# Performance work log

Measured on AMD Instinct MI355X. Metric: run time of the kernel, lower is better.

The kernel has to match this reference:

```python
import jax, jax.numpy as jnp
import numpy as np

N_CH = 62
F_DIM = 16
T_DIM = 32
B_DIM = 256
N_NODES = B_DIM * N_CH  # 15872
E_DIM = 200000
SEQ = T_DIM * F_DIM  # 512


def setup_inputs() -> dict:
    key = jax.random.key(0)
    ks = iter(jax.random.split(key, 40))
    s = 0.05
    inp = {}
    inp['x'] = jax.random.normal(next(ks), (N_NODES, F_DIM, T_DIM), dtype=jnp.float32)
    inp['edge_index'] = jax.random.randint(next(ks), (T_DIM, 2, E_DIM), 0, N_NODES, dtype=jnp.int64)
    inp['edge_weight'] = jax.random.uniform(next(ks), (T_DIM, E_DIM), dtype=jnp.float32)
    inp['batch'] = jax.random.randint(next(ks), (T_DIM, N_NODES), 0, B_DIM, dtype=jnp.int64)
    # ChebConv params (K=2): lins have no bias, single bias added at end
    for p in ['c1', 'c2']:
        inp[p + '_w0'] = jax.random.normal(next(ks), (F_DIM, F_DIM), dtype=jnp.float32) * s
        inp[p + '_w1'] = jax.random.normal(next(ks), (F_DIM, F_DIM), dtype=jnp.float32) * s
        inp[p + '_b'] = jnp.zeros((F_DIM,), jnp.float32)
    # LSTM params (torch gate order i,f,g,o); fold b_ih+b_hh into one bias
    for name, i_dim, h_dim in [('l1', N_CH, 64), ('l2', 64, 128), ('l3', 128, 256)]:
        inp[name + '_wih'] = jax.random.normal(next(ks), (4 * h_dim, i_dim), dtype=jnp.float32) * s
        inp[name + '_whh'] = jax.random.normal(next(ks), (4 * h_dim, h_dim), dtype=jnp.float32) * s
        inp[name + '_b'] = jnp.zeros((4 * h_dim,), jnp.float32)
    # MLP head
    for name, i_dim, o_dim in [('fc1', SEQ * 256, 256), ('fc2', 256, 128), ('fc3', 128, 64), ('fc4', 64, 4)]:
        inp[name + '_w'] = jax.random.normal(next(ks), (i_dim, o_dim), dtype=jnp.float32) * s
        inp[name + '_b'] = jnp.zeros((o_dim,), jnp.float32)
    return inp


def _cheb(x, src, dst, w, w0, w1, b):
    # PyG ChebConv K=2, sym norm, lambda_max=2: Tx1 = -D^{-1/2} A D^{-1/2} x
    n = x.shape[0]
    deg = jax.ops.segment_sum(w, src, num_segments=n)
    dinv = jnp.where(deg > 0, jax.lax.rsqrt(deg), 0.0)
    norm = -dinv[src] * w * dinv[dst]
    tx1 = jax.ops.segment_sum(norm[:, None] * x[src], dst, num_segments=n)
    return x @ w0 + tx1 @ w1 + b


def _lstm(x, wih, whh, b):
    # x: [B, S, I] -> [B, S, H], batch_first, zero init state
    bsz, _, _ = x.shape
    h_dim = whh.shape[1]
    xg = x @ wih.T + b  # precompute input gates [B, S, 4H]
    def step(carry, xt):
        h, c = carry
        g = xt + h @ whh.T
        i, f, gg, o = jnp.split(g, 4, axis=-1)
        c = jax.nn.sigmoid(f) * c + jax.nn.sigmoid(i) * jnp.tanh(gg)
        h = jax.nn.sigmoid(o) * jnp.tanh(c)
        return (h, c), h
    h0 = jnp.zeros((bsz, h_dim), x.dtype)
    _, hs = jax.lax.scan(step, (h0, h0), jnp.swapaxes(xg, 0, 1))
    return jnp.swapaxes(hs, 0, 1)


def reference(x, edge_index, edge_weight, batch,
              c1_w0, c1_w1, c1_b, c2_w0, c2_w1, c2_b,
              l1_wih, l1_whh, l1_b, l2_wih, l2_whh, l2_b, l3_wih, l3_whh, l3_b,
              fc1_w, fc1_b, fc2_w, fc2_b, fc3_w, fc3_b, fc4_w, fc4_b):
    def per_t(xt, ei, w):
        h = _cheb(xt, ei[0], ei[1], w, c1_w0, c1_w1, c1_b)
        h = jax.nn.leaky_relu(h, 0.01)
        return _cheb(h, ei[0], ei[1], w, c2_w0, c2_w1, c2_b)
    xt_first = jnp.moveaxis(x, -1, 0)  # [T, N, F]
    h = jax.vmap(per_t)(xt_first, edge_index, edge_weight)  # [T, N, F]
    xc = jnp.moveaxis(h, 0, -1)  # [N, F, T]
    xc = xc.reshape(B_DIM, N_CH, F_DIM, T_DIM)
    xc = jnp.transpose(xc, (0, 3, 2, 1))  # [B, T, F, 62]
    xc = xc.reshape(B_DIM, T_DIM * F_DIM, N_CH)  # [B, S, 62]
    h = _lstm(xc, l1_wih, l1_whh, l1_b)
    h = _lstm(h, l2_wih, l2_whh, l2_b)
    h = _lstm(h, l3_wih, l3_whh, l3_b)
    z = h.reshape(B_DIM, -1)  # [B, S*256]
    z = jax.nn.relu(z @ fc1_w + fc1_b)
    z = jax.nn.relu(z @ fc2_w + fc2_b)
    z = jax.nn.relu(z @ fc3_w + fc3_b)
    return z @ fc4_w + fc4_b
```

## Files before the change

### kernel.cpp

```cpp
#include <hip/hip_runtime.h>
#include <cstdint>
#include <cstddef>


#define T_DIM 32
#define F_DIMC 16
#define NNODE 15872
#define EDGES 200000
#define BATCH 256
#define SEQL 512
#define TN (T_DIM * NNODE)
#define TE (T_DIM * EDGES)

typedef unsigned short ushortT;
typedef __bf16 bf16_t;
typedef bf16_t bf16x8 __attribute__((ext_vector_type(8)));
typedef float f32x4 __attribute__((ext_vector_type(4)));

__device__ __forceinline__ ushortT f2bf(float f) {
  union { float f; unsigned u; } v; v.f = f;
  unsigned u = v.u;
  u += 0x7fffu + ((u >> 16) & 1u);
  return (ushortT)(u >> 16);
}
__device__ __forceinline__ float fsig(float x) { return 1.0f / (1.0f + __expf(-x)); }
__device__ __forceinline__ float ftanh(float x) {
  float e = __expf(2.0f * x);
  return 1.0f - 2.0f / (e + 1.0f);
}
#define PIN(v) asm volatile("" : "+v"(v))

__device__ __forceinline__ void bar_sync() {
  asm volatile("s_waitcnt lgkmcnt(0)\n\ts_barrier" ::: "memory");
  __builtin_amdgcn_sched_barrier(0);
}

__global__ void k_wprep(const float* __restrict__ w1i, const float* __restrict__ w1h,
                        const float* __restrict__ w2i, const float* __restrict__ w2h,
                        const float* __restrict__ w3i, const float* __restrict__ w3h,
                        ushortT* __restrict__ Wcat) {
  int id = blockIdx.x * 256 + threadIdx.x;
  if (id >= 524288) return;
  float v;
  if (id < 32768) {
    int g = id >> 7, k = id & 127;
    v = (k < 62) ? w1i[g * 62 + k] : ((k >= 64) ? w1h[g * 64 + (k - 64)] : 0.0f);
  } else if (id < 131072) {
    int j = id - 32768; int g = j / 192, k = j % 192;
    v = (k < 64) ? w2i[g * 64 + k] : w2h[g * 128 + (k - 64)];
  } else {
    int j = id - 131072; int g = j / 384, k = j % 384;
    v = (k < 128) ? w3i[g * 128 + k] : w3h[g * 256 + (k - 128)];
  }
  Wcat[id] = f2bf(v);
}

__global__ void k_transpose(const float* __restrict__ x, float* __restrict__ xt) {
  __shared__ float s[528];
  int n = blockIdx.x;
  int tid = threadIdx.x;
  for (int i = tid; i < 512; i += 256) {
    s[(i >> 5) * 33 + (i & 31)] = x[(size_t)n * 512 + i];
  }
  __syncthreads();
  for (int i = tid; i < 512; i += 256) {
    int t = i >> 4, f = i & 15;
    xt[((size_t)t * NNODE + n) * 16 + f] = s[f * 33 + t];
  }
}

__global__ __launch_bounds__(1024, 1) void k_hist(const int* __restrict__ ei,
                                                  const float* __restrict__ ew,
                                                  float* __restrict__ deg,
                                                  int* __restrict__ counts,
                                                  int* __restrict__ rank) {
  __shared__ float sdeg[NNODE];
  __shared__ int scnt[NNODE];
  int t = blockIdx.x;
  int tid = threadIdx.x;
  for (int i = tid; i < NNODE; i += 1024) { sdeg[i] = 0.0f; scnt[i] = 0; }
  __syncthreads();
  const int* srcp = ei + (size_t)(2 * t) * EDGES;
  const int* dstp = ei + (size_t)(2 * t + 1) * EDGES;
  const float* ewp = ew + (size_t)t * EDGES;
  int* rankp = rank + (size_t)t * EDGES;
  for (int e = tid; e < EDGES; e += 1024) {
    int src = srcp[e];
    int dst = dstp[e];
    float w = ewp[e];
    atomicAdd(&sdeg[src], w);
    rankp[e] = atomicAdd(&scnt[dst], 1);
  }
  __syncthreads();
  float* degp = deg + (size_t)t * NNODE;
  int* cntp = counts + (size_t)t * NNODE;
  for (int i = tid; i < NNODE; i += 1024) {
    degp[i] = sdeg[i];
    cntp[i] = scnt[i];
  }
}

__global__ void k_scanA(const int* __restrict__ counts, int* __restrict__ offs,
                        int* __restrict__ ctot, float* __restrict__ deg) {
  __shared__ int s[256];
  int tid = threadIdx.x;
  int gid = blockIdx.x * 256 + tid;
  float d = deg[gid];
  int v = counts[gid];
  s[tid] = v; __syncthreads();
  for (int off = 1; off < 256; off <<= 1) {
    int x = (tid >= off) ? s[tid - off] : 0;
    __syncthreads();
    s[tid] += x;
    __syncthreads();
  }
  offs[gid] = s[tid] - v;
  if (tid == 255) ctot[blockIdx.x] = s[255];
  deg[gid] = (d > 0.0f) ? rsqrtf(d) : 0.0f;
}

__global__ void k_scanB(const int* __restrict__ ctot, int* __restrict__ cbase) {
  __shared__ int s[256];
  int tid = threadIdx.x;
  int carry = 0;
  for (int c = 0; c < 8; ++c) {
    int i = c * 256 + tid;
    int v = (i < 1984) ? ctot[i] : 0;
    s[tid] = v; __syncthreads();
    for (int off = 1; off < 256; off <<= 1) {
      int x = (tid >= off) ? s[tid - off] : 0;
      __syncthreads();
      s[tid] += x;
      __syncthreads();
    }
    if (i < 1984) cbase[i] = carry + s[tid] - v;
    int tot = s[255];
    __syncthreads();
    carry += tot;
  }
}

__global__ void k_fill2(const int* __restrict__ ei, const float* __restrict__ ew,
                        const float* __restrict__ dinv, const int* __restrict__ offs,
                        const int* __restrict__ cbase, const int* __restrict__ rank,
                        int* __restrict__ csrs, float* __restrict__ csrn) {
  int id = blockIdx.x * 256 + threadIdx.x;
  if (id >= TE) return;
  int t = id / EDGES, e = id % EDGES;
  int src = ei[(size_t)(2 * t) * EDGES + e];
  int dst = ei[(size_t)(2 * t + 1) * EDGES + e];
  int idx = t * NNODE + dst;
  int pos = offs[idx] + cbase[idx >> 8] + rank[id];
  csrs[pos] = src;
  csrn[pos] = -dinv[t * NNODE + src] * ew[id] * dinv[idx];
}

__device__ __forceinline__ void fma4(float4& a, float sc, const float4 b) {
  a.x += sc * b.x; a.y += sc * b.y; a.z += sc * b.z; a.w += sc * b.w;
}

__global__ void k_gc(const float* __restrict__ in, const int* __restrict__ offs,
                     const int* __restrict__ cbase,
                     const int* __restrict__ csrs, const float* __restrict__ csrn,
                     const float* __restrict__ w0, const float* __restrict__ w1,
                     const float* __restrict__ bias, float* __restrict__ outF,
                     ushortT* __restrict__ outX, int mode) {
  __shared__ float sw0[256], sw1[256], sb[16];
  int tid = threadIdx.x;
  sw0[tid] = w0[tid];
  sw1[tid] = w1[tid];
  if (tid < 16) sb[tid] = bias[tid];
  __syncthreads();
  int idx = blockIdx.x * 256 + tid;
  if (idx >= TN) return;
  int t = idx / NNODE, n = idx % NNODE;
  const float4* rowp = (const float4*)(in + (size_t)idx * 16);
  float4 x0 = rowp[0], x1 = rowp[1], x2 = rowp[2], x3 = rowp[3];
  float4 a0 = {0, 0, 0, 0}, a1 = {0, 0, 0, 0}, a2 = {0, 0, 0, 0}, a3 = {0, 0, 0, 0};
  int beg = offs[idx] + cbase[idx >> 8];
  int end = (idx == TN - 1) ? TE : offs[idx + 1] + cbase[(idx + 1) >> 8];
  const float* base = in + (size_t)t * NNODE * 16;
  for (int p2 = beg; p2 < end; ++p2) {
    int s = csrs[p2];
    float nr = csrn[p2];
    const float4* rp = (const float4*)(base + (size_t)s * 16);
    fma4(a0, nr, rp[0]); fma4(a1, nr, rp[1]); fma4(a2, nr, rp[2]); fma4(a3, nr, rp[3]);
  }
  float xr[16], ar[16];
  *(float4*)&xr[0] = x0; *(float4*)&xr[4] = x1; *(float4*)&xr[8] = x2; *(float4*)&xr[12] = x3;
  *(float4*)&ar[0] = a0; *(float4*)&ar[4] = a1; *(float4*)&ar[8] = a2; *(float4*)&ar[12] = a3;
  float o[16];
#pragma unroll
  for (int j = 0; j < 16; ++j) o[j] = sb[j];
#pragma unroll
  for (int k = 0; k < 16; ++k) {
    float xv = xr[k], av = ar[k];
#pragma unroll
    for (int j = 0; j < 16; ++j) o[j] += xv * sw0[k * 16 + j] + av * sw1[k * 16 + j];
  }
  if (mode == 0) {
#pragma unroll
    for (int j = 0; j < 16; ++j) o[j] = (o[j] > 0.0f) ? o[j] : 0.01f * o[j];
    float4* op = (float4*)(outF + (size_t)idx * 16);
    op[0] = *(float4*)&o[0]; op[1] = *(float4*)&o[4];
    op[2] = *(float4*)&o[8]; op[3] = *(float4*)&o[12];
  } else {
    int bb = n / 62, ch = n % 62;
#pragma unroll
    for (int j = 0; j < 16; ++j)
      outX[((size_t)(bb * 512 + t * 16 + j)) * 64 + ch] = f2bf(o[j]);
    if (ch < 2) {
#pragma unroll
      for (int j = 0; j < 16; ++j)
        outX[((size_t)(bb * 512 + t * 16 + j)) * 64 + 62 + ch] = 0;
    }
  }
}

__global__ __launch_bounds__(512, 1) void k_lstm(const ushortT* __restrict__ xc,
                                                 const ushortT* __restrict__ Wcat,
                                                 const float* __restrict__ b1g,
                                                 const float* __restrict__ b2g,
                                                 const float* __restrict__ b3g,
                                                 ushortT* __restrict__ zbuf,
                                                 uint32_t* __restrict__ h2x,
                                                 uint32_t* __restrict__ xbuf) {
  __shared__ ushortT X1[2][16 * 72];
  __shared__ ushortT H1[2][16 * 72];
  __shared__ ushortT H2[2][16 * 136];
  __shared__ ushortT HS[2][16 * 136];
  __shared__ ushortT PS[2][16 * 136];
  __shared__ ushortT H2S[2][16 * 136];
  int tid = threadIdx.x;
  int wv = tid >> 6, lane = tid & 63;
  int col = lane & 15, koff = (lane >> 4) * 8, m = lane & 15;
  int bx = blockIdx.x;

  if (bx < 16) {
    int g = bx;
    int bg = g * 16;
    const ushortT* W1 = Wcat;
    const ushortT* W2 = Wcat + 32768;

    bf16x8 w1r[4][4];
    if (wv < 4) {
#pragma unroll
      for (int q = 0; q < 4; ++q)
#pragma unroll
        for (int k = 0; k < 4; ++k) {
          w1r[q][k] = *reinterpret_cast<const bf16x8*>(
              &W1[(size_t)(q * 64 + wv * 16 + col) * 128 + k * 32 + koff]);
          PIN(w1r[q][k]);
        }
    }
    bf16x8 w2r[4][6];
#pragma unroll
    for (int q = 0; q < 4; ++q)
#pragma unroll
      for (int k = 0; k < 6; ++k) {
        w2r[q][k] = *reinterpret_cast<const bf16x8*>(
            &W2[(size_t)(q * 128 + wv * 16 + col) * 192 + k * 32 + koff]);
        PIN(w2r[q][k]);
      }
    float b1v[4] = {0, 0, 0, 0}, b2v[4];
    if (wv < 4) {
#pragma unroll
      for (int q = 0; q < 4; ++q) b1v[q] = b1g[q * 64 + wv * 16 + col];
    }
#pragma unroll
    for (int q = 0; q < 4; ++q) b2v[q] = b2g[q * 128 + wv * 16 + col];

    float c1r[4] = {0, 0, 0, 0};
    float c2r[4] = {0, 0, 0, 0};

    for (int i = tid; i < 2 * 16 * 72; i += 512) { X1[0][i] = 0; H1[0][i] = 0; }
    for (int i = tid; i < 2 * 16 * 136; i += 512) H2[0][i] = 0;
    __syncthreads();
    uint4 xreg = {0, 0, 0, 0};
    {
      int tid2 = tid - 256;
      if (tid2 >= 0 && tid2 < 128) {
        int mm = tid2 >> 3, jj = (tid2 & 7) * 8;
        *(uint4*)&X1[0][mm * 72 + jj] =
            *(const uint4*)&xc[((size_t)(bg + mm) * 512 + 0) * 64 + jj];
        xreg = *(const uint4*)&xc[((size_t)(bg + mm) * 512 + 1) * 64 + jj];
      }
    }
    __syncthreads();

    uint32_t* h2g = h2x + (size_t)g * 512 * 2048;

    for (int t = 0; t < 512; ++t) {
      int pr = t & 1, pw = 1 - pr;
      if (wv < 4) {
        f32x4 acc[4] = {};
#pragma unroll
        for (int kt = 0; kt < 4; ++kt) {
          const ushortT* ap = (kt < 2) ? &X1[pr][m * 72 + kt * 32 + koff]
                                       : &H1[pr][m * 72 + (kt - 2) * 32 + koff];
          bf16x8 a = *reinterpret_cast<const bf16x8*>(ap);
#pragma unroll
          for (int q = 0; q < 4; ++q)
            acc[q] = __builtin_amdgcn_mfma_f32_16x16x32_bf16(a, w1r[q][kt], acc[q], 0, 0, 0);
        }
#pragma unroll
        for (int r = 0; r < 4; ++r) {
          int row = (lane >> 4) * 4 + r;
          int lc = wv * 16 + col;
          float gi = acc[0][r] + b1v[0];
          float gf = acc[1][r] + b1v[1];
          float gg = acc[2][r] + b1v[2];
          float go = acc[3][r] + b1v[3];
          float c = fsig(gf) * c1r[r] + fsig(gi) * ftanh(gg);
          float h = fsig(go) * ftanh(c);
          c1r[r] = c;
          H1[pw][row * 72 + lc] = f2bf(h);
        }
      } else {
        int tid2 = tid - 256;
        if (tid2 < 128) {
          int mm = tid2 >> 3, jj = (tid2 & 7) * 8;
          if (t + 1 < 512)
            *(uint4*)&X1[pw][mm * 72 + jj] = xreg;
          int tf = (t + 2 < 512) ? t + 2 : 511;
          xreg = *(const uint4*)&xc[((size_t)(bg + mm) * 512 + tf) * 64 + jj];
        }
      }
      bar_sync();
      {
        f32x4 acc[4] = {};
#pragma unroll
        for (int kt = 0; kt < 6; ++kt) {
          const ushortT* ap = (kt < 2) ? &H1[pw][m * 72 + kt * 32 + koff]
                                       : &H2[pr][m * 136 + (kt - 2) * 32 + koff];
          bf16x8 a = *reinterpret_cast<const bf16x8*>(ap);
#pragma unroll
          for (int q = 0; q < 4; ++q)
            acc[q] = __builtin_amdgcn_mfma_f32_16x16x32_bf16(a, w2r[q][kt], acc[q], 0, 0, 0);
        }
        uint32_t tag = ((uint32_t)(t + 1)) << 16;
#pragma unroll
        for (int r = 0; r < 4; ++r) {
          int row = (lane >> 4) * 4 + r;
          int lc = wv * 16 + col;
          float gi = acc[0][r] + b2v[0];
          float gf = acc[1][r] + b2v[1];
          float gg = acc[2][r] + b2v[2];
          float go = acc[3][r] + b2v[3];
          float c = fsig(gf) * c2r[r] + fsig(gi) * ftanh(gg);
          float h = fsig(go) * ftanh(c);
          c2r[r] = c;
          ushortT hb = f2bf(h);
          H2[pw][row * 136 + lc] = hb;
          __hip_atomic_store(&h2g[(size_t)t * 2048 + row * 128 + lc], tag | hb,
                             __ATOMIC_RELAXED, __HIP_MEMORY_SCOPE_AGENT);
        }
      }
      bar_sync();
    }
  } else {
    int bxx = bx - 16;
    int s = (bxx >> 3) & 1;
    int g = (bxx & 7) | ((bxx >> 4) << 3);
    int ps = 1 - s;
    int bg = g * 16;
    const ushortT* W3 = Wcat + 131072;

    bf16x8 wH[4][4], wO[4][4], wP[4][4];
#pragma unroll
    for (int q = 0; q < 4; ++q) {
      const ushortT* rw = &W3[(size_t)(q * 256 + s * 128 + wv * 16 + col) * 384];
#pragma unroll
      for (int j = 0; j < 4; ++j) {
        wH[q][j] = *reinterpret_cast<const bf16x8*>(&rw[j * 32 + koff]);
        wO[q][j] = *reinterpret_cast<const bf16x8*>(&rw[(4 + s * 4 + j) * 32 + koff]);
        wP[q][j] = *reinterpret_cast<const bf16x8*>(&rw[(4 + ps * 4 + j) * 32 + koff]);
        PIN(wH[q][j]); PIN(wO[q][j]); PIN(wP[q][j]);
      }
    }
    float b3v[4];
#pragma unroll
    for (int q = 0; q < 4; ++q) b3v[q] = b3g[q * 256 + s * 128 + wv * 16 + col];

    float c3r[4] = {0, 0, 0, 0};

    for (int i = tid; i < 2 * 16 * 136; i += 512) HS[0][i] = 0;
    __syncthreads();

    uint32_t* myslot = xbuf + (((size_t)g * 2 + s) * 2) * 2048;
    const uint32_t* pslot = xbuf + (((size_t)g * 2 + ps) * 2) * 2048;
    const uint32_t* h2g = h2x + (size_t)g * 512 * 2048;

    int prow = tid >> 5, pc0 = (tid & 31) * 4;

    {
      const uint32_t* hp = h2g + prow * 128 + pc0;
      uint32_t u0 = __hip_atomic_load(hp + 0, __ATOMIC_RELAXED, __HIP_MEMORY_SCOPE_AGENT);
      uint32_t u1 = __hip_atomic_load(hp + 1, __ATOMIC_RELAXED, __HIP_MEMORY_SCOPE_AGENT);
      uint32_t u2 = __hip_atomic_load(hp + 2, __ATOMIC_RELAXED, __HIP_MEMORY_SCOPE_AGENT);
      uint32_t u3 = __hip_atomic_load(hp + 3, __ATOMIC_RELAXED, __HIP_MEMORY_SCOPE_AGENT);
      for (;;) {
        bool ok = ((u0 >> 16) == 1u) & ((u1 >> 16) == 1u) &
                  ((u2 >> 16) == 1u) & ((u3 >> 16) == 1u);
        if (ok) break;
        u0 = __hip_atomic_load(hp + 0, __ATOMIC_RELAXED, __HIP_MEMORY_SCOPE_AGENT);
        u1 = __hip_atomic_load(hp + 1, __ATOMIC_RELAXED, __HIP_MEMORY_SCOPE_AGENT);
        u2 = __hip_atomic_load(hp + 2, __ATOMIC_RELAXED, __HIP_MEMORY_SCOPE_AGENT);
        u3 = __hip_atomic_load(hp + 3, __ATOMIC_RELAXED, __HIP_MEMORY_SCOPE_AGENT);
      }
      H2S[0][prow * 136 + pc0 + 0] = (ushortT)(u0 & 0xffffu);
      H2S[0][prow * 136 + pc0 + 1] = (ushortT)(u1 & 0xffffu);
      H2S[0][prow * 136 + pc0 + 2] = (ushortT)(u2 & 0xffffu);
      H2S[0][prow * 136 + pc0 + 3] = (ushortT)(u3 & 0xffffu);
    }
    __syncthreads();

    for (int t = 0; t < 512; ++t) {
      int prt = t & 1, pw = 1 - prt;
      const uint32_t* pb = pslot + (size_t)prt * 2048 + prow * 128 + pc0;
      uint32_t v0 = 0, v1 = 0, v2 = 0, v3 = 0;
      if (t > 0) {
        v0 = __hip_atomic_load(pb + 0, __ATOMIC_RELAXED, __HIP_MEMORY_SCOPE_AGENT);
        v1 = __hip_atomic_load(pb + 1, __ATOMIC_RELAXED, __HIP_MEMORY_SCOPE_AGENT);
        v2 = __hip_atomic_load(pb + 2, __ATOMIC_RELAXED, __HIP_MEMORY_SCOPE_AGENT);
        v3 = __hip_atomic_load(pb + 3, __ATOMIC_RELAXED, __HIP_MEMORY_SCOPE_AGENT);
      }
      const uint32_t* hp = h2g + (size_t)(t + 1) * 2048 + prow * 128 + pc0;
      uint32_t u0 = 0, u1 = 0, u2 = 0, u3 = 0;
      if (t < 511) {
        u0 = __hip_atomic_load(hp + 0, __ATOMIC_RELAXED, __HIP_MEMORY_SCOPE_AGENT);
        u1 = __hip_atomic_load(hp + 1, __ATOMIC_RELAXED, __HIP_MEMORY_SCOPE_AGENT);
        u2 = __hip_atomic_load(hp + 2, __ATOMIC_RELAXED, __HIP_MEMORY_SCOPE_AGENT);
        u3 = __hip_atomic_load(hp + 3, __ATOMIC_RELAXED, __HIP_MEMORY_SCOPE_AGENT);
      }
      __builtin_amdgcn_sched_barrier(0);
      f32x4 acc[4] = {};
#pragma unroll
      for (int kt = 0; kt < 4; ++kt) {
        bf16x8 a = *reinterpret_cast<const bf16x8*>(&H2S[prt][m * 136 + kt * 32 + koff]);
#pragma unroll
        for (int q = 0; q < 4; ++q)
          acc[q] = __builtin_amdgcn_mfma_f32_16x16x32_bf16(a, wH[q][kt], acc[q], 0, 0, 0);
      }
      if (t > 0) {
#pragma unroll
        for (int j = 0; j < 4; ++j) {
          bf16x8 a = *reinterpret_cast<const bf16x8*>(&HS[prt][m * 136 + j * 32 + koff]);
#pragma unroll
          for (int q = 0; q < 4; ++q)
            acc[q] = __builtin_amdgcn_mfma_f32_16x16x32_bf16(a, wO[q][j], acc[q], 0, 0, 0);
        }
        {
          uint32_t want = (uint32_t)t;
          while (((v0 >> 16) != want) | ((v1 >> 16) != want) |
                 ((v2 >> 16) != want) | ((v3 >> 16) != want)) {
            v0 = __hip_atomic_load(pb + 0, __ATOMIC_RELAXED, __HIP_MEMORY_SCOPE_AGENT);
            v1 = __hip_atomic_load(pb + 1, __ATOMIC_RELAXED, __HIP_MEMORY_SCOPE_AGENT);
            v2 = __hip_atomic_load(pb + 2, __ATOMIC_RELAXED, __HIP_MEMORY_SCOPE_AGENT);
            v3 = __hip_atomic_load(pb + 3, __ATOMIC_RELAXED, __HIP_MEMORY_SCOPE_AGENT);
          }
          PS[prt][prow * 136 + pc0 + 0] = (ushortT)(v0 & 0xffffu);
          PS[prt][prow * 136 + pc0 + 1] = (ushortT)(v1 & 0xffffu);
          PS[prt][prow * 136 + pc0 + 2] = (ushortT)(v2 & 0xffffu);
          PS[prt][prow * 136 + pc0 + 3] = (ushortT)(v3 & 0xffffu);
        }
        bar_sync();
#pragma unroll
        for (int j = 0; j < 4; ++j) {
          bf16x8 a = *reinterpret_cast<const bf16x8*>(&PS[prt][m * 136 + j * 32 + koff]);
#pragma unroll
          for (int q = 0; q < 4; ++q)
            acc[q] = __builtin_amdgcn_mfma_f32_16x16x32_bf16(a, wP[q][j], acc[q], 0, 0, 0);
        }
      }
      if (t < 511) {
        uint32_t want = (uint32_t)(t + 2);
        while (((u0 >> 16) != want) | ((u1 >> 16) != want) |
               ((u2 >> 16) != want) | ((u3 >> 16) != want)) {
          u0 = __hip_atomic_load(hp + 0, __ATOMIC_RELAXED, __HIP_MEMORY_SCOPE_AGENT);
          u1 = __hip_atomic_load(hp + 1, __ATOMIC_RELAXED, __HIP_MEMORY_SCOPE_AGENT);
          u2 = __hip_atomic_load(hp + 2, __ATOMIC_RELAXED, __HIP_MEMORY_SCOPE_AGENT);
          u3 = __hip_atomic_load(hp + 3, __ATOMIC_RELAXED, __HIP_MEMORY_SCOPE_AGENT);
        }
        H2S[pw][prow * 136 + pc0 + 0] = (ushortT)(u0 & 0xffffu);
        H2S[pw][prow * 136 + pc0 + 1] = (ushortT)(u1 & 0xffffu);
        H2S[pw][prow * 136 + pc0 + 2] = (ushortT)(u2 & 0xffffu);
        H2S[pw][prow * 136 + pc0 + 3] = (ushortT)(u3 & 0xffffu);
      }
      uint32_t* mw = myslot + (size_t)((t + 1) & 1) * 2048;
      ushortT hbs[4];
#pragma unroll
      for (int r = 0; r < 4; ++r) {
        int row = (lane >> 4) * 4 + r;
        int lc = wv * 16 + col;
        float gi = acc[0][r] + b3v[0];
        float gf = acc[1][r] + b3v[1];
        float gg = acc[2][r] + b3v[2];
        float go = acc[3][r] + b3v[3];
        float c = fsig(gf) * c3r[r] + fsig(gi) * ftanh(gg);
        float h = fsig(go) * ftanh(c);
        c3r[r] = c;
        hbs[r] = f2bf(h);
        __hip_atomic_store(mw + row * 128 + lc, ((uint32_t)(t + 1) << 16) | hbs[r],
                           __ATOMIC_RELAXED, __HIP_MEMORY_SCOPE_AGENT);
      }
      asm volatile("s_waitcnt vmcnt(0)" ::: "memory");
      __builtin_amdgcn_sched_barrier(0);
#pragma unroll
      for (int r = 0; r < 4; ++r) {
        int row = (lane >> 4) * 4 + r;
        int lc = wv * 16 + col;
        HS[pw][row * 136 + lc] = hbs[r];
        zbuf[((size_t)(bg + row) * 512 + t) * 256 + s * 128 + lc] = hbs[r];
      }
      bar_sync();
    }
  }
}

__global__ __launch_bounds__(256) void k_fc1(const ushortT* __restrict__ zbuf,
                                             const float* __restrict__ w,
                                             float* __restrict__ part) {
  __shared__ ushortT As[256 * 40];
  __shared__ ushortT Bs[64 * 40];
  int tid = threadIdx.x;
  int kb = blockIdx.x;
  int nb = blockIdx.y;
  int wv = tid >> 6, lane = tid & 63;
  int col = lane & 15, koff = (lane >> 4) * 8;
  int k0base = kb * 2048;
  f32x4 acc[4][4] = {};
  for (int kt = 0; kt < 64; ++kt) {
    int k0 = k0base + kt * 32;
    {
      const uint4* src = (const uint4*)(zbuf + (size_t)tid * 131072 + k0);
      uint4* dst = (uint4*)(As + tid * 40);
      dst[0] = src[0]; dst[1] = src[1]; dst[2] = src[2]; dst[3] = src[3];
    }
    {
      int kk = tid >> 3, j0 = (tid & 7) * 8;
      const float* srcw = w + (size_t)(k0 + kk) * 256 + nb * 64 + j0;
#pragma unroll
      for (int jj = 0; jj < 8; ++jj) Bs[(j0 + jj) * 40 + kk] = f2bf(srcw[jj]);
    }
    __syncthreads();
    bf16x8 bfr[4];
#pragma unroll
    for (int nt = 0; nt < 4; ++nt)
      bfr[nt] = *reinterpret_cast<const bf16x8*>(&Bs[(nt * 16 + col) * 40 + koff]);
#pragma unroll
    for (int mt = 0; mt < 4; ++mt) {
      bf16x8 afr = *reinterpret_cast<const bf16x8*>(&As[(wv * 64 + mt * 16 + col) * 40 + koff]);
#pragma unroll
      for (int nt = 0; nt < 4; ++nt)
        acc[mt][nt] = __builtin_amdgcn_mfma_f32_16x16x32_bf16(afr, bfr[nt], acc[mt][nt], 0, 0, 0);
    }
    __syncthreads();
  }
#pragma unroll
  for (int mt = 0; mt < 4; ++mt)
#pragma unroll
    for (int nt = 0; nt < 4; ++nt)
#pragma unroll
      for (int r = 0; r < 4; ++r) {
        int m = wv * 64 + mt * 16 + (lane >> 4) * 4 + r;
        int n = nb * 64 + nt * 16 + col;
        part[(size_t)kb * 65536 + m * 256 + n] = acc[mt][nt][r];
      }
}

__global__ void k_fc1red(const float* __restrict__ part, const float* __restrict__ b,
                         float* __restrict__ out) {
  int id4 = blockIdx.x * 256 + threadIdx.x;
  if (id4 >= 16384) return;
  float4 s = {0.0f, 0.0f, 0.0f, 0.0f};
  for (int kb = 0; kb < 64; ++kb) {
    float4 v = *(const float4*)&part[(size_t)kb * 65536 + id4 * 4];
    s.x += v.x; s.y += v.y; s.z += v.z; s.w += v.w;
  }
  int n0 = (id4 * 4) & 255;
  s.x = fmaxf(s.x + b[n0 + 0], 0.0f);
  s.y = fmaxf(s.y + b[n0 + 1], 0.0f);
  s.z = fmaxf(s.z + b[n0 + 2], 0.0f);
  s.w = fmaxf(s.w + b[n0 + 3], 0.0f);
  *(float4*)&out[id4 * 4] = s;
}

__global__ void k_fcv(const float* __restrict__ in, const float* __restrict__ w,
                      const float* __restrict__ b, float* __restrict__ out,
                      int K, int Nn, int doRelu) {
  int id = blockIdx.x * 256 + threadIdx.x;
  int m = id / Nn, n = id % Nn;
  float s = b[n];
  for (int k = 0; k < K; ++k) s += in[m * K + k] * w[k * Nn + n];
  if (doRelu) s = fmaxf(s, 0.0f);
  out[id] = s;
}

extern "C" void kernel_launch(void* const* d_in, const int* in_sizes, int n_in,
                              void* d_out, int out_size, void* d_ws, size_t ws_size,
                              hipStream_t stream) {
  (void)in_sizes; (void)n_in; (void)out_size; (void)ws_size;
  const float* x    = (const float*)d_in[0];
  const int* ei     = (const int*)d_in[1];
  const float* ew   = (const float*)d_in[2];
  const float* c1w0 = (const float*)d_in[4];
  const float* c1w1 = (const float*)d_in[5];
  const float* c1b  = (const float*)d_in[6];
  const float* c2w0 = (const float*)d_in[7];
  const float* c2w1 = (const float*)d_in[8];
  const float* c2b  = (const float*)d_in[9];
  const float* l1wi = (const float*)d_in[10];
  const float* l1wh = (const float*)d_in[11];
  const float* l1b  = (const float*)d_in[12];
  const float* l2wi = (const float*)d_in[13];
  const float* l2wh = (const float*)d_in[14];
  const float* l2b  = (const float*)d_in[15];
  const float* l3wi = (const float*)d_in[16];
  const float* l3wh = (const float*)d_in[17];
  const float* l3b  = (const float*)d_in[18];
  const float* fc1w = (const float*)d_in[19];
  const float* fc1b = (const float*)d_in[20];
  const float* fc2w = (const float*)d_in[21];
  const float* fc2b = (const float*)d_in[22];
  const float* fc3w = (const float*)d_in[23];
  const float* fc3b = (const float*)d_in[24];
  const float* fc4w = (const float*)d_in[25];
  const float* fc4b = (const float*)d_in[26];
  float* out = (float*)d_out;

  char* p = (char*)d_ws;
  auto alloc = [&](size_t bytes) { void* r = (void*)p; p += (bytes + 255) & ~(size_t)255; return r; };
  float* xt      = (float*)alloc(32505856);
  float* h1buf   = (float*)alloc(32505856);
  float* dinv    = (float*)alloc(2031616);
  int* counts    = (int*)alloc(2031616);
  int* offs      = (int*)alloc(2031616);
  int* fillc     = (int*)alloc(2031616);
  int* ctot      = (int*)alloc(8192);
  int* cbase     = (int*)alloc(8192);
  int* csrs      = (int*)alloc(25600000);
  float* csrn    = (float*)alloc(25600000);
  ushortT* xc    = (ushortT*)alloc(16777216);
  ushortT* Wcat  = (ushortT*)alloc(1048576);
  ushortT* zbuf  = (ushortT*)alloc(67108864);
  float* part    = (float*)alloc(16777216);
  float* fo1     = (float*)alloc(262144);
  float* fo2     = (float*)alloc(131072);
  float* fo3     = (float*)alloc(65536);
  uint32_t* xbuf = (uint32_t*)alloc(524288);
  (void)fillc;
  int* rank = (int*)h1buf;
  uint32_t* h2x = (uint32_t*)xt;


  k_wprep<<<2048, 256, 0, stream>>>(l1wi, l1wh, l2wi, l2wh, l3wi, l3wh, Wcat);
  k_transpose<<<15872, 256, 0, stream>>>(x, xt);
  k_hist<<<32, 1024, 0, stream>>>(ei, ew, dinv, counts, rank);
  k_scanA<<<1984, 256, 0, stream>>>(counts, offs, ctot, dinv);
  k_scanB<<<1, 256, 0, stream>>>(ctot, cbase);
  k_fill2<<<25000, 256, 0, stream>>>(ei, ew, dinv, offs, cbase, rank, csrs, csrn);
  k_gc<<<1984, 256, 0, stream>>>(xt, offs, cbase, csrs, csrn, c1w0, c1w1, c1b, h1buf, nullptr, 0);
  k_gc<<<1984, 256, 0, stream>>>(h1buf, offs, cbase, csrs, csrn, c2w0, c2w1, c2b, nullptr, xc, 1);
  hipMemsetAsync(h2x, 0, 67108864, stream);
  k_lstm<<<48, 512, 0, stream>>>(xc, Wcat, l1b, l2b, l3b, zbuf, h2x, xbuf);
  k_fc1<<<dim3(64, 4), 256, 0, stream>>>(zbuf, fc1w, part);
  k_fc1red<<<64, 256, 0, stream>>>(part, fc1b, fo1);
  k_fcv<<<128, 256, 0, stream>>>(fo1, fc2w, fc2b, fo2, 256, 128, 1);
  k_fcv<<<64, 256, 0, stream>>>(fo2, fc3w, fc3b, fo3, 128, 64, 1);
  k_fcv<<<4, 256, 0, stream>>>(fo3, fc4w, fc4b, out, 64, 4, 0);
}
```

Before: 3.189 ms.

## Split per-timestep histogram across eight edge segments with merge pass

```diff
diff --git a/kernel.cpp b/kernel.cpp
--- a/kernel.cpp
+++ b/kernel.cpp
@@ -11,6 +11,7 @@
 #define SEQL 512
 #define TN (T_DIM * NNODE)
 #define TE (T_DIM * EDGES)
+#define ESEG 25000
 
 typedef unsigned short ushortT;
 typedef __bf16 bf16_t;
@@ -69,14 +70,15 @@
   }
 }
 
-__global__ __launch_bounds__(1024, 1) void k_hist(const int* __restrict__ ei,
-                                                  const float* __restrict__ ew,
-                                                  float* __restrict__ deg,
-                                                  int* __restrict__ counts,
-                                                  int* __restrict__ rank) {
+__global__ __launch_bounds__(1024, 1) void k_hist8(const int* __restrict__ ei,
+                                                   const float* __restrict__ ew,
+                                                   float* __restrict__ pdeg,
+                                                   int* __restrict__ pcnt,
+                                                   int* __restrict__ rank) {
   __shared__ float sdeg[NNODE];
   __shared__ int scnt[NNODE];
-  int t = blockIdx.x;
+  int t = blockIdx.x >> 3;
+  int b = blockIdx.x & 7;
   int tid = threadIdx.x;
   for (int i = tid; i < NNODE; i += 1024) { sdeg[i] = 0.0f; scnt[i] = 0; }
   __syncthreads();
@@ -84,7 +86,8 @@
   const int* dstp = ei + (size_t)(2 * t + 1) * EDGES;
   const float* ewp = ew + (size_t)t * EDGES;
   int* rankp = rank + (size_t)t * EDGES;
-  for (int e = tid; e < EDGES; e += 1024) {
+  int e0 = b * ESEG, e1 = e0 + ESEG;
+  for (int e = e0 + tid; e < e1; e += 1024) {
     int src = srcp[e];
     int dst = dstp[e];
     float w = ewp[e];
@@ -92,12 +95,34 @@
     rankp[e] = atomicAdd(&scnt[dst], 1);
   }
   __syncthreads();
-  float* degp = deg + (size_t)t * NNODE;
-  int* cntp = counts + (size_t)t * NNODE;
+  float* pd = pdeg + (size_t)blockIdx.x * NNODE;
+  int* pc = pcnt + (size_t)blockIdx.x * NNODE;
   for (int i = tid; i < NNODE; i += 1024) {
-    degp[i] = sdeg[i];
-    cntp[i] = scnt[i];
-  }
+    pd[i] = sdeg[i];
+    pc[i] = scnt[i];
+  }
+}
+
+__global__ void k_merge(const float* __restrict__ pdeg, const int* __restrict__ pcnt,
+                        float* __restrict__ deg, int* __restrict__ counts,
+                        int* __restrict__ bko) {
+  int gid = blockIdx.x * 256 + threadIdx.x;
+  if (gid >= TN) return;
+  int t = gid / NNODE, n = gid % NNODE;
+  int base = t * 8;
+  float d = 0.0f;
+  int s = 0;
+  int pref[8];
+#pragma unroll
+  for (int b = 0; b < 8; ++b) {
+    pref[b] = s;
+    d += pdeg[(size_t)(base + b) * NNODE + n];
+    s += pcnt[(size_t)(base + b) * NNODE + n];
+  }
+#pragma unroll
+  for (int b = 0; b < 8; ++b) bko[(size_t)gid * 8 + b] = pref[b];
+  deg[gid] = d;
+  counts[gid] = s;
 }
 
 __global__ void k_scanA(const int* __restrict__ counts, int* __restrict__ offs,
@@ -142,7 +167,8 @@
 
 __global__ void k_fill2(const int* __restrict__ ei, const float* __restrict__ ew,
                         const float* __restrict__ dinv, const int* __restrict__ offs,
-                        const int* __restrict__ cbase, const int* __restrict__ rank,
+                        const int* __restrict__ cbase, const int* __restrict__ bko,
+                        const int* __restrict__ rank,
                         int* __restrict__ csrs, float* __restrict__ csrn) {
   int id = blockIdx.x * 256 + threadIdx.x;
   if (id >= TE) return;
@@ -150,7 +176,8 @@
   int src = ei[(size_t)(2 * t) * EDGES + e];
   int dst = ei[(size_t)(2 * t + 1) * EDGES + e];
   int idx = t * NNODE + dst;
-  int pos = offs[idx] + cbase[idx >> 8] + rank[id];
+  int seg = e / ESEG;
+  int pos = offs[idx] + cbase[idx >> 8] + bko[(size_t)idx * 8 + seg] + rank[id];
   csrs[pos] = src;
   csrn[pos] = -dinv[t * NNODE + src] * ew[id] * dinv[idx];
 }
@@ -652,14 +679,18 @@
   (void)fillc;
   int* rank = (int*)h1buf;
   uint32_t* h2x = (uint32_t*)xt;
+  float* pdeg = (float*)zbuf;
+  int* pcnt = (int*)((char*)zbuf + 16777216);
+  int* bko = (int*)((char*)zbuf + 35127296);
 
 
   k_wprep<<<2048, 256, 0, stream>>>(l1wi, l1wh, l2wi, l2wh, l3wi, l3wh, Wcat);
   k_transpose<<<15872, 256, 0, stream>>>(x, xt);
-  k_hist<<<32, 1024, 0, stream>>>(ei, ew, dinv, counts, rank);
+  k_hist8<<<256, 1024, 0, stream>>>(ei, ew, pdeg, pcnt, rank);
+  k_merge<<<1984, 256, 0, stream>>>(pdeg, pcnt, dinv, counts, bko);
   k_scanA<<<1984, 256, 0, stream>>>(counts, offs, ctot, dinv);
   k_scanB<<<1, 256, 0, stream>>>(ctot, cbase);
-  k_fill2<<<25000, 256, 0, stream>>>(ei, ew, dinv, offs, cbase, rank, csrs, csrn);
+  k_fill2<<<25000, 256, 0, stream>>>(ei, ew, dinv, offs, cbase, bko, rank, csrs, csrn);
   k_gc<<<1984, 256, 0, stream>>>(xt, offs, cbase, csrs, csrn, c1w0, c1w1, c1b, h1buf, nullptr, 0);
   k_gc<<<1984, 256, 0, stream>>>(h1buf, offs, cbase, csrs, csrn, c2w0, c2w1, c2b, nullptr, xc, 1);
   hipMemsetAsync(h2x, 0, 67108864, stream);
```

Result: faster. 3.008 ms (-5.7%).
